# Kernel optimization log

Measured on AMD Instinct MI355X. Metric: run time of the kernel, lower is better.

The kernel has to match this reference:

```python
import jax, jax.numpy as jnp
import numpy as np

N, E, B = 20000, 320000, 128      # nodes, edges, graphs in batch
H = 32                            # h_atom == n_bond
N_ATOM_FEAT, N_BOND_FEAT = 64, 16
N_LAYERS = 2


def setup_inputs() -> dict:
    key = jax.random.key(0)
    ks = jax.random.split(key, 12)
    s = 0.1
    return dict(
        n_feat=jax.random.normal(ks[0], (N, N_ATOM_FEAT), jnp.float32),
        e_feat=jax.random.normal(ks[1], (E, N_BOND_FEAT), jnp.float32),
        src=jax.random.randint(ks[2], (E,), 0, N, jnp.int32),
        dst=jax.random.randint(ks[3], (E,), 0, N, jnp.int32),
        graph_ids=jnp.sort(jax.random.randint(ks[4], (N,), 0, B, jnp.int32)),
        W_atom=jax.random.normal(ks[5], (N_ATOM_FEAT, H), jnp.float32) * s,
        b_atom=jnp.zeros((H,), jnp.float32),
        W_bond=jax.random.normal(ks[6], (N_BOND_FEAT, H), jnp.float32) * s,
        b_bond=jnp.zeros((H,), jnp.float32),
        W_e1=jax.random.normal(ks[7], (H, H), jnp.float32) * s,
        b_e1=jnp.zeros((H,), jnp.float32),
        W_e2=jax.random.normal(ks[8], (H, H * H), jnp.float32) * s,
        b_e2=jnp.zeros((H * H,), jnp.float32),
        W_ih=jax.random.normal(ks[9], (3 * H, H), jnp.float32) * s,
        W_hh=jax.random.normal(ks[10], (3 * H, H), jnp.float32) * s,
        b_ih=jnp.zeros((3 * H,), jnp.float32),
        b_hh=jnp.zeros((3 * H,), jnp.float32),
    )


def _gru_step(x, h, W_ih, W_hh, b_ih, b_hh):
    # torch nn.GRU single-cell update (seq_len=1)
    gi = x @ W_ih.T + b_ih
    gh = h @ W_hh.T + b_hh
    ir, iz, ig = jnp.split(gi, 3, axis=-1)
    hr, hz, hg = jnp.split(gh, 3, axis=-1)
    r = jax.nn.sigmoid(ir + hr)
    z = jax.nn.sigmoid(iz + hz)
    n = jnp.tanh(ig + r * hg)
    return (1.0 - z) * n + z * h


def reference(n_feat, e_feat, src, dst, graph_ids, W_atom, b_atom, W_bond, b_bond,
              W_e1, b_e1, W_e2, b_e2, W_ih, W_hh, b_ih, b_hh):
    # dense embeddings
    h = n_feat @ W_atom + b_atom              # [N, H]
    h_bond = e_feat @ W_bond + b_bond         # [E, H]
    # NNConv edge network -> per-edge weight matrix [E, H_in, H_out]
    ew = jax.nn.relu(h_bond @ W_e1 + b_e1) @ W_e2 + b_e2
    W_edge = ew.reshape(E, H, H)
    # in-degree for mean aggregation (zero in-degree -> 0, like DGL mean)
    deg = jax.ops.segment_sum(jnp.ones((E,), h.dtype), dst, num_segments=N)
    inv_deg = 1.0 / jnp.maximum(deg, 1.0)
    for _ in range(N_LAYERS):
        msg = jnp.einsum('ei,eio->eo', h[src], W_edge)                  # [E, H]
        agg = jax.ops.segment_sum(msg, dst, num_segments=N) * inv_deg[:, None]
        m = jax.nn.relu(agg)
        h = _gru_step(m, h, W_ih, W_hh, b_ih, b_hh)
    # dgl.mean_nodes: per-graph mean of node states
    gsum = jax.ops.segment_sum(h, graph_ids, num_segments=B)            # [B, H]
    gcnt = jax.ops.segment_sum(jnp.ones((N,), h.dtype), graph_ids, num_segments=B)
    return gsum / jnp.maximum(gcnt, 1.0)[:, None]
```

## Files before the change

kernel.cpp:

```cpp
#include <hip/hip_runtime.h>
#include <hip/hip_fp16.h>
#include <math.h>

#define N_NODES 20000
#define N_EDGES 320000
#define NB 128
#define H 32
#define AF 64
#define BF 16
#define SCB 79
#define SCP 20224

typedef _Float16 f16x2 __attribute__((ext_vector_type(2)));

__device__ __forceinline__ float fast_sigmoid(float x) {
  return 1.0f / (1.0f + __expf(-x));
}
__device__ __forceinline__ float fast_tanh(float x) {
  float e2 = __expf(2.0f * x);
  return 1.0f - 2.0f / (e2 + 1.0f);
}
__device__ __forceinline__ unsigned int pk2(float a, float b) {
  union { f16x2 h; unsigned int u; } p;
  p.h[0] = (_Float16)a;
  p.h[1] = (_Float16)b;
  return p.u;
}
__device__ __forceinline__ float uph(unsigned int u, int hi) {
  union { unsigned int u; f16x2 h; } x; x.u = u;
  return hi ? (float)x.h[1] : (float)x.h[0];
}
__device__ __forceinline__ float dot2(unsigned int a, unsigned int b, float c) {
  union { unsigned int u; f16x2 h; } ua, ub;
  ua.u = a; ub.u = b;
#if __has_builtin(__builtin_amdgcn_fdot2)
  return __builtin_amdgcn_fdot2(ua.h, ub.h, c, false);
#else
  return c + (float)ua.h[0] * (float)ub.h[0] + (float)ua.h[1] * (float)ub.h[1];
#endif
}

__global__ __launch_bounds__(256) void embed_nodes(const float* __restrict__ nf,
    const float* __restrict__ W, const float* __restrict__ b, float* __restrict__ h) {
  __shared__ float Ws[AF * H];
  __shared__ float nfs[8][AF];
  int tid = threadIdx.x;
  for (int v = tid; v < AF * H; v += 256) Ws[v] = W[v];
  int n0 = blockIdx.x * 8;
  for (int v = tid; v < 8 * AF; v += 256) {
    int nl = v / AF, k = v % AF;
    int n = n0 + nl;
    nfs[nl][k] = (n < N_NODES) ? nf[n * AF + k] : 0.0f;
  }
  __syncthreads();
  int nl = tid / H, o = tid % H;
  int n = n0 + nl;
  if (n >= N_NODES) return;
  float acc = b[o];
#pragma unroll
  for (int k = 0; k < AF; k++) acc += nfs[nl][k] * Ws[k * H + o];
  h[n * H + o] = acc;
}

__global__ __launch_bounds__(256) void pack_We2(const float* __restrict__ We2,
    const float* __restrict__ be2, unsigned int* __restrict__ Wp) {
  int idx = blockIdx.x * 256 + threadIdx.x;
  if (idx >= 33 * 512) return;
  int j = idx >> 9, r = idx & 511;
  int ip = r >> 5, o = r & 31;
  const float* src = (j < 32) ? (We2 + (size_t)j * (H * H)) : be2;
  Wp[idx] = pk2(src[(2 * ip) * H + o], src[(2 * ip + 1) * H + o]);
}

__global__ void hist2(const int* __restrict__ src, const int* __restrict__ dst,
                      int* __restrict__ hsrc, int* __restrict__ hdst) {
  int e = blockIdx.x * 256 + threadIdx.x;
  if (e < N_EDGES) {
    atomicAdd(&hsrc[src[e]], 1);
    atomicAdd(&hdst[dst[e]], 1);
  }
}

__global__ __launch_bounds__(256) void scan_partial(const int* __restrict__ hist_s,
    const int* __restrict__ hist_d, int* __restrict__ part, int* __restrict__ bsum) {
  __shared__ int wsums[4];
  int which = blockIdx.y;
  const int* __restrict__ hh = which ? hist_d : hist_s;
  int i = blockIdx.x * 256 + threadIdx.x;
  int v = (i < N_NODES) ? hh[i] : 0;
  int lane = threadIdx.x & 63, wid = threadIdx.x >> 6;
  int incl = v;
#pragma unroll
  for (int off = 1; off < 64; off <<= 1) {
    int t = __shfl_up(incl, off, 64);
    if (lane >= off) incl += t;
  }
  if (lane == 63) wsums[wid] = incl;
  __syncthreads();
  int woff = 0;
#pragma unroll
  for (int w = 0; w < 4; w++) if (w < wid) woff += wsums[w];
  part[which * SCP + i] = woff + incl - v;
  if (threadIdx.x == 0)
    bsum[which * SCB + blockIdx.x] = wsums[0] + wsums[1] + wsums[2] + wsums[3];
}

__global__ __launch_bounds__(256) void scan_tops(int* __restrict__ bsum,
    const int* __restrict__ gid, int* __restrict__ gstart) {
  __shared__ int s[2 * SCB];
  int tid = threadIdx.x;
  if (tid < 2 * SCB) s[tid] = bsum[tid];
  if (tid < NB) {
    int g = tid;
    int lo = 0, hi = N_NODES;
    while (lo < hi) { int mid = (lo + hi) >> 1; if (gid[mid] < g) lo = mid + 1; else hi = mid; }
    gstart[g] = lo;
    if (g == 0) gstart[NB] = N_NODES;
  }
  __syncthreads();
  if (tid < 2) {
    int run = 0;
    for (int b = 0; b < SCB; b++) { int t = s[tid * SCB + b]; s[tid * SCB + b] = run; run += t; }
  }
  __syncthreads();
  if (tid < 2 * SCB) bsum[tid] = s[tid];
}

__global__ __launch_bounds__(256) void scan_final(const int* __restrict__ part,
    const int* __restrict__ bsum, const int* __restrict__ hist_d,
    int* __restrict__ cur_s, int* __restrict__ cur_d,
    int* __restrict__ seg_s, int* __restrict__ seg_d, float* __restrict__ inv_deg) {
  int which = blockIdx.y;
  int i = blockIdx.x * 256 + threadIdx.x;
  if (i >= N_NODES) return;
  int ex = part[which * SCP + i] + bsum[which * SCB + blockIdx.x];
  if (which == 0) {
    cur_s[i] = ex; seg_s[i] = ex;
    if (i == 0) seg_s[N_NODES] = N_EDGES;
  } else {
    cur_d[i] = ex; seg_d[i] = ex;
    inv_deg[i] = 1.0f / fmaxf((float)hist_d[i], 1.0f);
    if (i == 0) seg_d[N_NODES] = N_EDGES;
  }
}

__global__ void scatter2_fast(const int* __restrict__ src, const int* __restrict__ dst,
    int* __restrict__ cur_s, int* __restrict__ cur_d,
    int* __restrict__ pos_s, int* __restrict__ dpos) {
  int e = blockIdx.x * 256 + threadIdx.x;
  if (e >= N_EDGES) return;
  int s = src[e], d = dst[e];
  int ps = atomicAdd(&cur_s[s], 1);
  int pd = atomicAdd(&cur_d[d], 1);
  dpos[ps] = pd;
  pos_s[e] = ps;
}

__global__ void scatter2_full(const int* __restrict__ src, const int* __restrict__ dst,
    int* __restrict__ cur_s, int* __restrict__ cur_d,
    int* __restrict__ src_s, int* __restrict__ dst_s,
    int* __restrict__ pos_s, int* __restrict__ dpos) {
  int e = blockIdx.x * 256 + threadIdx.x;
  if (e >= N_EDGES) return;
  int s = src[e], d = dst[e];
  int ps = atomicAdd(&cur_s[s], 1);
  int pd = atomicAdd(&cur_d[d], 1);
  src_s[ps] = s;
  dst_s[ps] = d;
  dpos[ps] = pd;
  pos_s[e] = ps;
}

__global__ __launch_bounds__(256) void edge_r(const float* __restrict__ ef,
    const float* __restrict__ Wb, const float* __restrict__ bb,
    const float* __restrict__ We1, const float* __restrict__ be1,
    const int* __restrict__ pos_s, unsigned int* __restrict__ rh) {
  __shared__ float Wbs[BF * H];
  __shared__ unsigned int W1p[16 * H];
  __shared__ float efs[32 * 20];
  __shared__ unsigned int hbp[32 * 20];
  int tid = threadIdx.x;
  for (int v = tid; v < BF * H; v += 256) Wbs[v] = Wb[v];
  for (int v = tid; v < 16 * H; v += 256) {
    int jp = v >> 5, o = v & 31;
    W1p[v] = pk2(We1[(2 * jp) * H + o], We1[(2 * jp + 1) * H + o]);
  }
  int e0 = blockIdx.x * 32;
  if (tid < 128) {
    float4 d = ((const float4*)(ef + (size_t)e0 * BF))[tid];
    ((float4*)(efs + (tid >> 2) * 20))[tid & 3] = d;
  }
  __syncthreads();
  int el = tid >> 3, oq = tid & 7;
  const float4* Wb4 = (const float4*)Wbs;
  const float4* efv = (const float4*)(efs + el * 20);
  float4 hb = ((const float4*)bb)[oq];
#pragma unroll
  for (int kq = 0; kq < 4; kq++) {
    float4 e4 = efv[kq];
    float4 w;
    w = Wb4[(kq * 4 + 0) * 8 + oq];
    hb.x += e4.x * w.x; hb.y += e4.x * w.y; hb.z += e4.x * w.z; hb.w += e4.x * w.w;
    w = Wb4[(kq * 4 + 1) * 8 + oq];
    hb.x += e4.y * w.x; hb.y += e4.y * w.y; hb.z += e4.y * w.z; hb.w += e4.y * w.w;
    w = Wb4[(kq * 4 + 2) * 8 + oq];
    hb.x += e4.z * w.x; hb.y += e4.z * w.y; hb.z += e4.z * w.z; hb.w += e4.z * w.w;
    w = Wb4[(kq * 4 + 3) * 8 + oq];
    hb.x += e4.w * w.x; hb.y += e4.w * w.y; hb.z += e4.w * w.z; hb.w += e4.w * w.w;
  }
  ((uint2*)(hbp + el * 20))[oq] = make_uint2(pk2(hb.x, hb.y), pk2(hb.z, hb.w));
  __syncthreads();
  float4 acc = ((const float4*)be1)[oq];
  const uint4* hb4 = (const uint4*)(hbp + el * 20);
#pragma unroll
  for (int q = 0; q < 4; q++) {
    uint4 hp = hb4[q];
    uint4 w;
    w = ((const uint4*)(W1p + (4 * q + 0) * H))[oq];
    acc.x = dot2(hp.x, w.x, acc.x); acc.y = dot2(hp.x, w.y, acc.y);
    acc.z = dot2(hp.x, w.z, acc.z); acc.w = dot2(hp.x, w.w, acc.w);
    w = ((const uint4*)(W1p + (4 * q + 1) * H))[oq];
    acc.x = dot2(hp.y, w.x, acc.x); acc.y = dot2(hp.y, w.y, acc.y);
    acc.z = dot2(hp.y, w.z, acc.z); acc.w = dot2(hp.y, w.w, acc.w);
    w = ((const uint4*)(W1p + (4 * q + 2) * H))[oq];
    acc.x = dot2(hp.z, w.x, acc.x); acc.y = dot2(hp.z, w.y, acc.y);
    acc.z = dot2(hp.z, w.z, acc.z); acc.w = dot2(hp.z, w.w, acc.w);
    w = ((const uint4*)(W1p + (4 * q + 3) * H))[oq];
    acc.x = dot2(hp.w, w.x, acc.x); acc.y = dot2(hp.w, w.y, acc.y);
    acc.z = dot2(hp.w, w.z, acc.z); acc.w = dot2(hp.w, w.w, acc.w);
  }
  acc.x = fmaxf(acc.x, 0.0f); acc.y = fmaxf(acc.y, 0.0f);
  acc.z = fmaxf(acc.z, 0.0f); acc.w = fmaxf(acc.w, 0.0f);
  int ps = pos_s[e0 + el];
  uint2 st;
  st.x = pk2(acc.x, acc.y);
  st.y = pk2(acc.z, acc.w);
  ((uint2*)(rh + (size_t)ps * 16))[oq] = st;
}

__global__ __launch_bounds__(256) void compute_T_fused(const float* __restrict__ h,
    const unsigned int* __restrict__ Wp,
    unsigned int* __restrict__ Th, float* __restrict__ hbias) {
  __shared__ unsigned int Wall[9 * 512];
  __shared__ unsigned int hp[32 * 17];
  int tid = threadIdx.x;
  int n0 = blockIdx.x * 32;
  int jb = blockIdx.y;
  int nslice = (jb == 3) ? 9 : 8;
  const uint4* Wsrc = (const uint4*)(Wp + (size_t)jb * 8 * 512);
#pragma unroll
  for (int v = 0; v < 4; v++) ((uint4*)Wall)[tid + v * 256] = Wsrc[tid + v * 256];
  if (jb == 3 && tid < 128)
    ((uint4*)(Wall + 8 * 512))[tid] = ((const uint4*)(Wp + 32 * 512))[tid];
  for (int v = tid; v < 512; v += 256) {
    int nl = v >> 4, ip = v & 15;
    float2 hv = ((const float2*)(h + (size_t)(n0 + nl) * H))[ip];
    hp[nl * 17 + ip] = pk2(hv.x, hv.y);
  }
  __syncthreads();
  int nl = tid >> 3, oq = tid & 7;
  unsigned int hreg[16];
#pragma unroll
  for (int ip = 0; ip < 16; ip++) hreg[ip] = hp[nl * 17 + ip];
  int n = n0 + nl;
  float4 pacc = make_float4(0.f, 0.f, 0.f, 0.f);
  for (int jj = 0; jj < nslice; jj++) {
    const uint4* W4 = (const uint4*)(Wall + jj * 512);
    float4 acc = make_float4(0.f, 0.f, 0.f, 0.f);
#pragma unroll
    for (int ip = 0; ip < 16; ip++) {
      unsigned int hpv = hreg[ip];
      uint4 w = W4[ip * 8 + oq];
      acc.x = dot2(hpv, w.x, acc.x);
      acc.y = dot2(hpv, w.y, acc.y);
      acc.z = dot2(hpv, w.z, acc.z);
      acc.w = dot2(hpv, w.w, acc.w);
    }
    int j = jb * 8 + jj;
    if (j < H) {
      if (jj & 1) {
        uint4 st;
        st.x = pk2(pacc.x, acc.x);
        st.y = pk2(pacc.y, acc.y);
        st.z = pk2(pacc.z, acc.z);
        st.w = pk2(pacc.w, acc.w);
        ((uint4*)(Th + (size_t)n * 512 + (j >> 1) * 32))[oq] = st;
      } else {
        pacc = acc;
      }
    } else {
      ((float4*)(hbias + (size_t)n * H))[oq] = acc;
    }
  }
}

__global__ __launch_bounds__(256) void edge_msg_seg(const unsigned int* __restrict__ rh,
    const unsigned int* __restrict__ Th, const float* __restrict__ hbias,
    const int* __restrict__ seg_s, const int* __restrict__ dpos,
    unsigned int* __restrict__ msg_h) {
  __shared__ unsigned int Ts[8 * 512];
  __shared__ float hb[8 * H];
  __shared__ int sseg[9];
  int tid = threadIdx.x;
  int n0 = blockIdx.x * 8;
  const uint4* Tg = (const uint4*)(Th + (size_t)n0 * 512);
#pragma unroll
  for (int v = 0; v < 4; v++) ((uint4*)Ts)[tid + v * 256] = Tg[tid + v * 256];
  hb[tid] = hbias[(size_t)n0 * H + tid];
  if (tid < 9) sseg[tid] = seg_s[n0 + tid];
  __syncthreads();
  int lane = tid & 63, wid = tid >> 6;
  int el = lane >> 3, t = lane & 7;
  for (int s = 0; s < 8; s++) {
    int a = sseg[s], bnd = sseg[s + 1];
    if (a >= bnd) continue;
    const unsigned int* Trow = Ts + s * 512;
    uint4 tw[16];
#pragma unroll
    for (int jp = 0; jp < 16; jp++) tw[jp] = ((const uint4*)(Trow + jp * 32))[t];
    float4 hbv = ((const float4*)(hb + s * H))[t];
    int ww = (wid + s) & 3;
    for (int base = a + ww * 8; base < bnd; base += 32) {
      int e = base + el;
      bool valid = (e < bnd);
      int pd = 0;
      unsigned int rr[16];
#pragma unroll
      for (int k = 0; k < 16; k++) rr[k] = 0u;
      if (valid) {
        pd = dpos[e];
        const uint4* rp = (const uint4*)(rh + (size_t)e * 16);
        *(uint4*)(&rr[0])  = rp[0];
        *(uint4*)(&rr[4])  = rp[1];
        *(uint4*)(&rr[8])  = rp[2];
        *(uint4*)(&rr[12]) = rp[3];
      }
      float4 acc = hbv;
#pragma unroll
      for (int jp = 0; jp < 16; jp++) {
        unsigned int rj = rr[jp];
        uint4 w = tw[jp];
        acc.x = dot2(rj, w.x, acc.x);
        acc.y = dot2(rj, w.y, acc.y);
        acc.z = dot2(rj, w.z, acc.z);
        acc.w = dot2(rj, w.w, acc.w);
      }
      if (valid) {
        uint2 st;
        st.x = pk2(acc.x, acc.y);
        st.y = pk2(acc.z, acc.w);
        ((uint2*)(msg_h + (size_t)pd * 16))[t] = st;
      }
    }
  }
}

__global__ __launch_bounds__(256) void edge_msg_atomic(const unsigned int* __restrict__ rh,
    const unsigned int* __restrict__ Th, const float* __restrict__ hbias,
    const int* __restrict__ src_s, const int* __restrict__ dst_s,
    float* __restrict__ agg) {
  int tid = threadIdx.x;
  int e0 = blockIdx.x * 32;
  int el = tid >> 3, t = tid & 7;
  int e = e0 + el;
  int s = src_s[e], d = dst_s[e];
  uint2 ru2 = ((const uint2*)(rh + (size_t)e * 16))[t];
  float4 acc = ((const float4*)(hbias + (size_t)s * H))[t];
  const unsigned int* Trow = Th + (size_t)s * 512;
#pragma unroll
  for (int jp = 0; jp < 16; jp++) {
    unsigned int mine = (jp & 1) ? ru2.y : ru2.x;
    unsigned int rj = (unsigned int)__shfl((int)mine, jp >> 1, 8);
    uint4 tw = ((const uint4*)(Trow + jp * 32))[t];
    acc.x = dot2(rj, tw.x, acc.x);
    acc.y = dot2(rj, tw.y, acc.y);
    acc.z = dot2(rj, tw.z, acc.z);
    acc.w = dot2(rj, tw.w, acc.w);
  }
  float* ap = agg + (size_t)d * H + t * 4;
  atomicAdd(ap + 0, acc.x);
  atomicAdd(ap + 1, acc.y);
  atomicAdd(ap + 2, acc.z);
  atomicAdd(ap + 3, acc.w);
}

__global__ __launch_bounds__(256) void seg_gru(const unsigned int* __restrict__ msg_h,
    const int* __restrict__ seg_d, const float* __restrict__ invdeg,
    const float* __restrict__ Wih, const float* __restrict__ Whh,
    const float* __restrict__ bih, const float* __restrict__ bhh,
    float* __restrict__ h) {
  __shared__ float Wis[3 * H][H + 1];
  __shared__ float Whs[3 * H][H + 1];
  __shared__ float xs[8][H + 1];
  __shared__ float hsm[8][H + 1];
  int tid = threadIdx.x;
  for (int v = tid; v < 3 * H * H; v += 256) {
    int k = v / H, i = v % H;
    Wis[k][i] = Wih[v];
    Whs[k][i] = Whh[v];
  }
  int node = tid >> 5, o = tid & 31;
  int n = blockIdx.x * 8 + node;
  int a = seg_d[n], bseg = seg_d[n + 1];
  int q = o & 3, g = o >> 2;
  float acc[8];
#pragma unroll
  for (int k = 0; k < 8; k++) acc[k] = 0.0f;
  int nrows = bseg - a;
#pragma unroll 2
  for (int p = g; p < nrows; p += 8) {
    uint4 m = ((const uint4*)(msg_h + (size_t)(a + p) * 16))[q];
    acc[0] += uph(m.x, 0); acc[1] += uph(m.x, 1);
    acc[2] += uph(m.y, 0); acc[3] += uph(m.y, 1);
    acc[4] += uph(m.z, 0); acc[5] += uph(m.z, 1);
    acc[6] += uph(m.w, 0); acc[7] += uph(m.w, 1);
  }
#pragma unroll
  for (int k = 0; k < 8; k++) {
    acc[k] += __shfl_xor(acc[k], 4, 32);
    acc[k] += __shfl_xor(acc[k], 8, 32);
    acc[k] += __shfl_xor(acc[k], 16, 32);
  }
  float idg = invdeg[n];
  if (g == 0) {
#pragma unroll
    for (int k = 0; k < 8; k++)
      xs[node][8 * q + k] = fmaxf(acc[k] * idg, 0.0f);
  }
  float hval = h[(size_t)n * H + o];
  hsm[node][o] = hval;
  __syncthreads();
  float gi0 = bih[o], gi1 = bih[H + o], gi2 = bih[2 * H + o];
  float gh0 = bhh[o], gh1 = bhh[H + o], gh2 = bhh[2 * H + o];
#pragma unroll
  for (int i = 0; i < H; i++) {
    float xi = xs[node][i], hi_ = hsm[node][i];
    gi0 += xi * Wis[o][i];
    gh0 += hi_ * Whs[o][i];
    gi1 += xi * Wis[H + o][i];
    gh1 += hi_ * Whs[H + o][i];
    gi2 += xi * Wis[2 * H + o][i];
    gh2 += hi_ * Whs[2 * H + o][i];
  }
  float rg = fast_sigmoid(gi0 + gh0);
  float zg = fast_sigmoid(gi1 + gh1);
  float ng = fast_tanh(gi2 + rg * gh2);
  h[(size_t)n * H + o] = (1.0f - zg) * ng + zg * hval;
}

__global__ __launch_bounds__(256) void gru_update(const float* __restrict__ agg,
    const float* __restrict__ invdeg, const float* __restrict__ Wih,
    const float* __restrict__ Whh, const float* __restrict__ bih,
    const float* __restrict__ bhh, float* __restrict__ h) {
  __shared__ float Wis[3 * H][H + 1];
  __shared__ float Whs[3 * H][H + 1];
  __shared__ float xs[8][H + 1];
  __shared__ float hsm[8][H + 1];
  int tid = threadIdx.x;
  for (int v = tid; v < 3 * H * H; v += 256) {
    int k = v / H, i = v % H;
    Wis[k][i] = Wih[v];
    Whs[k][i] = Whh[v];
  }
  int node = tid >> 5, o = tid & 31;
  int n = blockIdx.x * 8 + node;
  xs[node][o] = fmaxf(agg[(size_t)n * H + o] * invdeg[n], 0.0f);
  float hval = h[(size_t)n * H + o];
  hsm[node][o] = hval;
  __syncthreads();
  float gi0 = bih[o], gi1 = bih[H + o], gi2 = bih[2 * H + o];
  float gh0 = bhh[o], gh1 = bhh[H + o], gh2 = bhh[2 * H + o];
#pragma unroll
  for (int i = 0; i < H; i++) {
    float xi = xs[node][i], hi_ = hsm[node][i];
    gi0 += xi * Wis[o][i];
    gh0 += hi_ * Whs[o][i];
    gi1 += xi * Wis[H + o][i];
    gh1 += hi_ * Whs[H + o][i];
    gi2 += xi * Wis[2 * H + o][i];
    gh2 += hi_ * Whs[2 * H + o][i];
  }
  float rg = fast_sigmoid(gi0 + gh0);
  float zg = fast_sigmoid(gi1 + gh1);
  float ng = fast_tanh(gi2 + rg * gh2);
  h[(size_t)n * H + o] = (1.0f - zg) * ng + zg * hval;
}

__global__ __launch_bounds__(256) void readout_graph(const float* __restrict__ h,
    const int* __restrict__ gstart, float* __restrict__ out) {
  __shared__ float red[8][H + 1];
  int g = blockIdx.x;
  int a = gstart[g], b = gstart[g + 1];
  int r = threadIdx.x >> 5, o = threadIdx.x & 31;
  float s = 0.0f;
  for (int n = a + r; n < b; n += 8) s += h[(size_t)n * H + o];
  red[r][o] = s;
  __syncthreads();
  if (r == 0) {
    float t = 0.0f;
#pragma unroll
    for (int k = 0; k < 8; k++) t += red[k][o];
    out[g * H + o] = t / fmaxf((float)(b - a), 1.0f);
  }
}

extern "C" void kernel_launch(void* const* d_in, const int* in_sizes, int n_in,
                              void* d_out, int out_size, void* d_ws, size_t ws_size,
                              hipStream_t stream) {
  const float* n_feat = (const float*)d_in[0];
  const float* e_feat = (const float*)d_in[1];
  const int*   src    = (const int*)d_in[2];
  const int*   dst    = (const int*)d_in[3];
  const int*   gid    = (const int*)d_in[4];
  const float* W_atom = (const float*)d_in[5];
  const float* b_atom = (const float*)d_in[6];
  const float* W_bond = (const float*)d_in[7];
  const float* b_bond = (const float*)d_in[8];
  const float* W_e1   = (const float*)d_in[9];
  const float* b_e1   = (const float*)d_in[10];
  const float* W_e2   = (const float*)d_in[11];
  const float* b_e2   = (const float*)d_in[12];
  const float* W_ih   = (const float*)d_in[13];
  const float* W_hh   = (const float*)d_in[14];
  const float* b_ih   = (const float*)d_in[15];
  const float* b_hh   = (const float*)d_in[16];
  float* out = (float*)d_out;

  char* ws = (char*)d_ws;
  size_t off = 0;
  float*        h      = (float*)(ws + off); off += (size_t)N_NODES * H * 4;
  unsigned int* rh     = (unsigned int*)(ws + off); off += (size_t)N_EDGES * 16 * 4;
  unsigned int* Th     = (unsigned int*)(ws + off); off += (size_t)N_NODES * 512 * 4;
  float*        hbias  = (float*)(ws + off); off += (size_t)N_NODES * H * 4;
  unsigned int* Wp     = (unsigned int*)(ws + off); off += (size_t)33 * 512 * 4;
  int*   hist_s = (int*)(ws + off);   off += (size_t)N_NODES * 4;
  int*   hist_d = (int*)(ws + off);   off += (size_t)N_NODES * 4;
  int*   cur_s  = (int*)(ws + off);   off += (size_t)N_NODES * 4;
  int*   cur_d  = (int*)(ws + off);   off += (size_t)N_NODES * 4;
  int*   seg_s  = (int*)(ws + off);   off += (size_t)(N_NODES + 1) * 4;
  int*   seg_d  = (int*)(ws + off);   off += (size_t)(N_NODES + 1) * 4;
  float* invdeg = (float*)(ws + off); off += (size_t)N_NODES * 4;
  int*   part   = (int*)(ws + off);   off += (size_t)2 * SCP * 4;
  int*   bsum   = (int*)(ws + off);   off += (size_t)2 * SCB * 4;
  int*   src_s  = (int*)(ws + off);   off += (size_t)N_EDGES * 4;
  int*   dst_s  = (int*)(ws + off);   off += (size_t)N_EDGES * 4;
  int*   dpos   = (int*)(ws + off);   off += (size_t)N_EDGES * 4;
  int*   gstart = (int*)(ws + off);   off += (size_t)(NB + 1) * 4;
  float* agg    = (float*)(ws + off); off += (size_t)N_NODES * H * 4;
  unsigned int* msg_h = (unsigned int*)(ws + off); off += (size_t)N_EDGES * 16 * 4;
  int use_msg = (ws_size >= off) ? 1 : 0;
  int* pos_s = (int*)Th;

  embed_nodes<<<N_NODES / 8, 256, 0, stream>>>(n_feat, W_atom, b_atom, h);
  pack_We2<<<(33 * 512 + 255) / 256, 256, 0, stream>>>(W_e2, b_e2, Wp);

  hipMemsetAsync(hist_s, 0, (size_t)2 * N_NODES * 4, stream);
  hist2<<<(N_EDGES + 255) / 256, 256, 0, stream>>>(src, dst, hist_s, hist_d);
  {
    dim3 gs(SCB, 2);
    scan_partial<<<gs, 256, 0, stream>>>(hist_s, hist_d, part, bsum);
    scan_tops<<<1, 256, 0, stream>>>(bsum, gid, gstart);
    scan_final<<<gs, 256, 0, stream>>>(part, bsum, hist_d, cur_s, cur_d,
                                       seg_s, seg_d, invdeg);
  }
  if (use_msg) {
    scatter2_fast<<<(N_EDGES + 255) / 256, 256, 0, stream>>>(src, dst, cur_s, cur_d,
                                                             pos_s, dpos);
  } else {
    scatter2_full<<<(N_EDGES + 255) / 256, 256, 0, stream>>>(src, dst, cur_s, cur_d,
                                                             src_s, dst_s, pos_s, dpos);
  }

  edge_r<<<N_EDGES / 32, 256, 0, stream>>>(e_feat, W_bond, b_bond, W_e1, b_e1,
                                           pos_s, rh);

  for (int layer = 0; layer < 2; layer++) {
    dim3 gT(N_NODES / 32, 4);
    compute_T_fused<<<gT, 256, 0, stream>>>(h, Wp, Th, hbias);
    if (use_msg) {
      edge_msg_seg<<<N_NODES / 8, 256, 0, stream>>>(rh, Th, hbias, seg_s,
                                                    dpos, msg_h);
      seg_gru<<<N_NODES / 8, 256, 0, stream>>>(msg_h, seg_d, invdeg,
                                               W_ih, W_hh, b_ih, b_hh, h);
    } else {
      hipMemsetAsync(agg, 0, (size_t)N_NODES * H * 4, stream);
      edge_msg_atomic<<<N_EDGES / 32, 256, 0, stream>>>(rh, Th, hbias, src_s, dst_s,
                                                        agg);
      gru_update<<<N_NODES / 8, 256, 0, stream>>>(agg, invdeg,
                                                  W_ih, W_hh, b_ih, b_hh, h);
    }
  }

  readout_graph<<<NB, 256, 0, stream>>>(h, gstart, out);
}
```

Before: 338.8 us.

## Fuse per-node T computation into edge message kernel and merge prep kernels

Computes each node's projected weight matrix T and bias directly in shared memory inside the edge message kernel, so the Th/hbias round trip through global memory and the separate compute_T launch per layer are gone. Node embedding, We2 packing and histogram zeroing are also merged into one prep launch, which removes two launches and a memset. In exchange, every edge block reloads the packed We2 weights (64 KB per block) and recomputes T for its 8 nodes, which adds register pressure and L2 traffic. The empty-segment skip is also tightened per wave.

```diff
diff --git a/kernel.cpp b/kernel.cpp
--- a/kernel.cpp
+++ b/kernel.cpp
@@ -10,6 +10,9 @@
 #define BF 16
 #define SCB 79
 #define SCP 20224
+#define EMB_BLOCKS 2500
+#define PACK_BLOCKS 66
+#define ZERO_BLOCKS 16
 
 typedef _Float16 f16x2 __attribute__((ext_vector_type(2)));
 
@@ -40,36 +43,40 @@
 #endif
 }
 
-__global__ __launch_bounds__(256) void embed_nodes(const float* __restrict__ nf,
-    const float* __restrict__ W, const float* __restrict__ b, float* __restrict__ h) {
-  __shared__ float Ws[AF * H];
-  __shared__ float nfs[8][AF];
-  int tid = threadIdx.x;
-  for (int v = tid; v < AF * H; v += 256) Ws[v] = W[v];
-  int n0 = blockIdx.x * 8;
-  for (int v = tid; v < 8 * AF; v += 256) {
-    int nl = v / AF, k = v % AF;
+__global__ __launch_bounds__(256) void prep(const float* __restrict__ nf,
+    const float* __restrict__ W, const float* __restrict__ b, float* __restrict__ h,
+    const float* __restrict__ We2, const float* __restrict__ be2,
+    unsigned int* __restrict__ Wp, int* __restrict__ hist2buf) {
+  int blk = blockIdx.x;
+  int tid = threadIdx.x;
+  if (blk < EMB_BLOCKS) {
+    __shared__ float Ws[AF * H];
+    __shared__ float nfs[8][AF];
+    for (int v = tid; v < AF * H; v += 256) Ws[v] = W[v];
+    int n0 = blk * 8;
+    for (int v = tid; v < 8 * AF; v += 256) {
+      int nl = v / AF, k = v % AF;
+      nfs[nl][k] = nf[(size_t)(n0 + nl) * AF + k];
+    }
+    __syncthreads();
+    int nl = tid / H, o = tid % H;
     int n = n0 + nl;
-    nfs[nl][k] = (n < N_NODES) ? nf[n * AF + k] : 0.0f;
-  }
-  __syncthreads();
-  int nl = tid / H, o = tid % H;
-  int n = n0 + nl;
-  if (n >= N_NODES) return;
-  float acc = b[o];
-#pragma unroll
-  for (int k = 0; k < AF; k++) acc += nfs[nl][k] * Ws[k * H + o];
-  h[n * H + o] = acc;
-}
-
-__global__ __launch_bounds__(256) void pack_We2(const float* __restrict__ We2,
-    const float* __restrict__ be2, unsigned int* __restrict__ Wp) {
-  int idx = blockIdx.x * 256 + threadIdx.x;
-  if (idx >= 33 * 512) return;
-  int j = idx >> 9, r = idx & 511;
-  int ip = r >> 5, o = r & 31;
-  const float* src = (j < 32) ? (We2 + (size_t)j * (H * H)) : be2;
-  Wp[idx] = pk2(src[(2 * ip) * H + o], src[(2 * ip + 1) * H + o]);
+    float acc = b[o];
+#pragma unroll
+    for (int k = 0; k < AF; k++) acc += nfs[nl][k] * Ws[k * H + o];
+    h[(size_t)n * H + o] = acc;
+  } else if (blk < EMB_BLOCKS + PACK_BLOCKS) {
+    int idx = (blk - EMB_BLOCKS) * 256 + tid;
+    if (idx < 33 * 512) {
+      int j = idx >> 9, r = idx & 511;
+      int ip = r >> 5, o = r & 31;
+      const float* src = (j < 32) ? (We2 + (size_t)j * (H * H)) : be2;
+      Wp[idx] = pk2(src[(2 * ip) * H + o], src[(2 * ip + 1) * H + o]);
+    }
+  } else {
+    int idx = (blk - EMB_BLOCKS - PACK_BLOCKS) * 256 + tid;
+    for (int i = idx; i < 2 * N_NODES; i += ZERO_BLOCKS * 256) hist2buf[i] = 0;
+  }
 }
 
 __global__ void hist2(const int* __restrict__ src, const int* __restrict__ dst,
@@ -238,6 +245,110 @@
   ((uint2*)(rh + (size_t)ps * 16))[oq] = st;
 }
 
+__global__ __launch_bounds__(256) void edge_msg_T(const float* __restrict__ h,
+    const unsigned int* __restrict__ Wp, const unsigned int* __restrict__ rh,
+    const int* __restrict__ seg_s, const int* __restrict__ dpos,
+    unsigned int* __restrict__ msg_h) {
+  __shared__ unsigned int Ts[8 * 512];
+  __shared__ unsigned int hp[8 * 16];
+  __shared__ float hb[8 * H];
+  __shared__ int sseg[9];
+  int tid = threadIdx.x;
+  int n0 = blockIdx.x * 8;
+  if (tid < 128) {
+    int nl = tid >> 4, ip = tid & 15;
+    float2 hv = ((const float2*)(h + (size_t)(n0 + nl) * H))[ip];
+    hp[nl * 16 + ip] = pk2(hv.x, hv.y);
+  }
+  if (tid < 9) sseg[tid] = seg_s[n0 + tid];
+  __syncthreads();
+  {
+    int jp = tid >> 4, oh = tid & 15;
+    uint2 w0[16], w1[16];
+    const unsigned int* W0 = Wp + (size_t)(2 * jp) * 512 + 2 * oh;
+    const unsigned int* W1 = Wp + (size_t)(2 * jp + 1) * 512 + 2 * oh;
+#pragma unroll
+    for (int ip = 0; ip < 16; ip++) {
+      w0[ip] = *(const uint2*)(W0 + ip * 32);
+      w1[ip] = *(const uint2*)(W1 + ip * 32);
+    }
+#pragma unroll
+    for (int nl = 0; nl < 8; nl++) {
+      uint4 h0 = ((const uint4*)(hp + nl * 16))[0];
+      uint4 h1 = ((const uint4*)(hp + nl * 16))[1];
+      uint4 h2 = ((const uint4*)(hp + nl * 16))[2];
+      uint4 h3 = ((const uint4*)(hp + nl * 16))[3];
+      unsigned int hr[16] = {h0.x, h0.y, h0.z, h0.w, h1.x, h1.y, h1.z, h1.w,
+                             h2.x, h2.y, h2.z, h2.w, h3.x, h3.y, h3.z, h3.w};
+      float t00 = 0.f, t01 = 0.f, t10 = 0.f, t11 = 0.f;
+#pragma unroll
+      for (int ip = 0; ip < 16; ip++) {
+        unsigned int hpv = hr[ip];
+        t00 = dot2(hpv, w0[ip].x, t00);
+        t01 = dot2(hpv, w0[ip].y, t01);
+        t10 = dot2(hpv, w1[ip].x, t10);
+        t11 = dot2(hpv, w1[ip].y, t11);
+      }
+      ((uint2*)(Ts + nl * 512 + jp * 32 + 2 * oh))[0] =
+          make_uint2(pk2(t00, t10), pk2(t01, t11));
+    }
+  }
+  {
+    int nl = tid >> 5, o = tid & 31;
+    const unsigned int* Wb32 = Wp + (size_t)32 * 512 + o;
+    float acc = 0.f;
+#pragma unroll
+    for (int ip = 0; ip < 16; ip++)
+      acc = dot2(hp[nl * 16 + ip], Wb32[ip * 32], acc);
+    hb[nl * H + o] = acc;
+  }
+  __syncthreads();
+  int lane = tid & 63, wid = tid >> 6;
+  int el = lane >> 3, t = lane & 7;
+  for (int s = 0; s < 8; s++) {
+    int a = sseg[s], bnd = sseg[s + 1];
+    int ww = (wid + s) & 3;
+    if (a + ww * 8 >= bnd) continue;
+    const unsigned int* Trow = Ts + s * 512;
+    uint4 tw[16];
+#pragma unroll
+    for (int jp = 0; jp < 16; jp++) tw[jp] = ((const uint4*)(Trow + jp * 32))[t];
+    float4 hbv = ((const float4*)(hb + s * H))[t];
+    for (int base = a + ww * 8; base < bnd; base += 32) {
+      int e = base + el;
+      bool valid = (e < bnd);
+      int pd = 0;
+      unsigned int rr[16];
+#pragma unroll
+      for (int k = 0; k < 16; k++) rr[k] = 0u;
+      if (valid) {
+        pd = dpos[e];
+        const uint4* rp = (const uint4*)(rh + (size_t)e * 16);
+        *(uint4*)(&rr[0])  = rp[0];
+        *(uint4*)(&rr[4])  = rp[1];
+        *(uint4*)(&rr[8])  = rp[2];
+        *(uint4*)(&rr[12]) = rp[3];
+      }
+      float4 acc = hbv;
+#pragma unroll
+      for (int jp = 0; jp < 16; jp++) {
+        unsigned int rj = rr[jp];
+        uint4 w = tw[jp];
+        acc.x = dot2(rj, w.x, acc.x);
+        acc.y = dot2(rj, w.y, acc.y);
+        acc.z = dot2(rj, w.z, acc.z);
+        acc.w = dot2(rj, w.w, acc.w);
+      }
+      if (valid) {
+        uint2 st;
+        st.x = pk2(acc.x, acc.y);
+        st.y = pk2(acc.z, acc.w);
+        ((uint2*)(msg_h + (size_t)pd * 16))[t] = st;
+      }
+    }
+  }
+}
+
 __global__ __launch_bounds__(256) void compute_T_fused(const float* __restrict__ h,
     const unsigned int* __restrict__ Wp,
     unsigned int* __restrict__ Th, float* __restrict__ hbias) {
@@ -290,67 +401,6 @@
       }
     } else {
       ((float4*)(hbias + (size_t)n * H))[oq] = acc;
-    }
-  }
-}
-
-__global__ __launch_bounds__(256) void edge_msg_seg(const unsigned int* __restrict__ rh,
-    const unsigned int* __restrict__ Th, const float* __restrict__ hbias,
-    const int* __restrict__ seg_s, const int* __restrict__ dpos,
-    unsigned int* __restrict__ msg_h) {
-  __shared__ unsigned int Ts[8 * 512];
-  __shared__ float hb[8 * H];
-  __shared__ int sseg[9];
-  int tid = threadIdx.x;
-  int n0 = blockIdx.x * 8;
-  const uint4* Tg = (const uint4*)(Th + (size_t)n0 * 512);
-#pragma unroll
-  for (int v = 0; v < 4; v++) ((uint4*)Ts)[tid + v * 256] = Tg[tid + v * 256];
-  hb[tid] = hbias[(size_t)n0 * H + tid];
-  if (tid < 9) sseg[tid] = seg_s[n0 + tid];
-  __syncthreads();
-  int lane = tid & 63, wid = tid >> 6;
-  int el = lane >> 3, t = lane & 7;
-  for (int s = 0; s < 8; s++) {
-    int a = sseg[s], bnd = sseg[s + 1];
-    if (a >= bnd) continue;
-    const unsigned int* Trow = Ts + s * 512;
-    uint4 tw[16];
-#pragma unroll
-    for (int jp = 0; jp < 16; jp++) tw[jp] = ((const uint4*)(Trow + jp * 32))[t];
-    float4 hbv = ((const float4*)(hb + s * H))[t];
-    int ww = (wid + s) & 3;
-    for (int base = a + ww * 8; base < bnd; base += 32) {
-      int e = base + el;
-      bool valid = (e < bnd);
-      int pd = 0;
-      unsigned int rr[16];
-#pragma unroll
-      for (int k = 0; k < 16; k++) rr[k] = 0u;
-      if (valid) {
-        pd = dpos[e];
-        const uint4* rp = (const uint4*)(rh + (size_t)e * 16);
-        *(uint4*)(&rr[0])  = rp[0];
-        *(uint4*)(&rr[4])  = rp[1];
-        *(uint4*)(&rr[8])  = rp[2];
-        *(uint4*)(&rr[12]) = rp[3];
-      }
-      float4 acc = hbv;
-#pragma unroll
-      for (int jp = 0; jp < 16; jp++) {
-        unsigned int rj = rr[jp];
-        uint4 w = tw[jp];
-        acc.x = dot2(rj, w.x, acc.x);
-        acc.y = dot2(rj, w.y, acc.y);
-        acc.z = dot2(rj, w.z, acc.z);
-        acc.w = dot2(rj, w.w, acc.w);
-      }
-      if (valid) {
-        uint2 st;
-        st.x = pk2(acc.x, acc.y);
-        st.y = pk2(acc.z, acc.w);
-        ((uint2*)(msg_h + (size_t)pd * 16))[t] = st;
-      }
     }
   }
 }
@@ -551,10 +601,9 @@
   int use_msg = (ws_size >= off) ? 1 : 0;
   int* pos_s = (int*)Th;
 
-  embed_nodes<<<N_NODES / 8, 256, 0, stream>>>(n_feat, W_atom, b_atom, h);
-  pack_We2<<<(33 * 512 + 255) / 256, 256, 0, stream>>>(W_e2, b_e2, Wp);
-
-  hipMemsetAsync(hist_s, 0, (size_t)2 * N_NODES * 4, stream);
+  prep<<<EMB_BLOCKS + PACK_BLOCKS + ZERO_BLOCKS, 256, 0, stream>>>(
+      n_feat, W_atom, b_atom, h, W_e2, b_e2, Wp, hist_s);
+
   hist2<<<(N_EDGES + 255) / 256, 256, 0, stream>>>(src, dst, hist_s, hist_d);
   {
     dim3 gs(SCB, 2);
@@ -575,14 +624,13 @@
                                            pos_s, rh);
 
   for (int layer = 0; layer < 2; layer++) {
-    dim3 gT(N_NODES / 32, 4);
-    compute_T_fused<<<gT, 256, 0, stream>>>(h, Wp, Th, hbias);
     if (use_msg) {
-      edge_msg_seg<<<N_NODES / 8, 256, 0, stream>>>(rh, Th, hbias, seg_s,
-                                                    dpos, msg_h);
+      edge_msg_T<<<N_NODES / 8, 256, 0, stream>>>(h, Wp, rh, seg_s, dpos, msg_h);
       seg_gru<<<N_NODES / 8, 256, 0, stream>>>(msg_h, seg_d, invdeg,
                                                W_ih, W_hh, b_ih, b_hh, h);
     } else {
+      dim3 gT(N_NODES / 32, 4);
+      compute_T_fused<<<gT, 256, 0, stream>>>(h, Wp, Th, hbias);
       hipMemsetAsync(agg, 0, (size_t)N_NODES * H * 4, stream);
       edge_msg_atomic<<<N_EDGES / 32, 256, 0, stream>>>(rh, Th, hbias, src_s, dst_s,
                                                         agg);
```

After: 304.6 us. 1.11x faster.
